# Performance work log

Hardware: AMD Instinct MI355X
Metric: run time of the kernel (lower is better)

## Reference

```python
import jax, jax.numpy as jnp
import numpy as np

GROUPS = 32
N_HEADS = 8
EPS = 1e-5


def setup_inputs() -> dict:
    key = jax.random.key(0)
    ks = jax.random.split(key, 4)
    B, C, H, W = 8, 512, 32, 32
    x = jax.random.normal(ks[0], (B, C, H, W), dtype=jnp.float32)
    norm_scale = jnp.ones((C,), jnp.float32)
    norm_bias = jnp.zeros((C,), jnp.float32)
    qkv_w = jax.random.normal(ks[1], (3 * C, C), jnp.float32) * (C ** -0.5)
    qkv_b = jnp.zeros((3 * C,), jnp.float32)
    proj_w = jax.random.normal(ks[2], (C, C), jnp.float32) * (C ** -0.5)
    proj_b = jnp.zeros((C,), jnp.float32)
    return {"x": x, "norm_scale": norm_scale, "norm_bias": norm_bias,
            "qkv_w": qkv_w, "qkv_b": qkv_b, "proj_w": proj_w, "proj_b": proj_b}


def reference(x, norm_scale, norm_bias, qkv_w, qkv_b, proj_w, proj_b):
    B, C, H, W = x.shape
    T = H * W
    xf = x.reshape(B, C, T)

    # GroupNorm32 (32 groups, computed in float32, affine)
    xg = xf.astype(jnp.float32).reshape(B, GROUPS, C // GROUPS, T)
    mean = xg.mean(axis=(2, 3), keepdims=True)
    var = xg.var(axis=(2, 3), keepdims=True)
    xn = ((xg - mean) * jax.lax.rsqrt(var + EPS)).reshape(B, C, T)
    xn = (xn * norm_scale[:, None] + norm_bias[:, None]).astype(x.dtype)

    # qkv: 1x1 conv1d == pointwise matmul -> [B, 3C, T]
    qkv = jnp.einsum('oc,bct->bot', qkv_w, xn) + qkv_b[:, None]

    # QKVAttentionLegacy: reshape to [B*H, 3*ch, T], split
    ch = C // N_HEADS
    qkv_h = qkv.reshape(B * N_HEADS, 3 * ch, T)
    q, k, v = qkv_h[:, :ch], qkv_h[:, ch:2 * ch], qkv_h[:, 2 * ch:]
    scale = ch ** -0.25
    weight = jnp.einsum('bct,bcs->bts', q * scale, k * scale)  # [B*H, T, T]
    weight = jax.nn.softmax(weight.astype(jnp.float32), axis=-1).astype(qkv.dtype)
    a = jnp.einsum('bts,bcs->bct', weight, v).reshape(B, C, T)

    # proj_out (1x1 conv) + residual
    h = jnp.einsum('oc,bct->bot', proj_w, a) + proj_b[:, None]
    return (xf + h).reshape(B, C, H, W)
```

## Files before the change

kernel.cpp:

```cpp
#include <hip/hip_runtime.h>
#include <hip/hip_bf16.h>
#include <stdint.h>

typedef unsigned short u16;
typedef unsigned int u32;
typedef __bf16 bf16x8 __attribute__((ext_vector_type(8)));
typedef float f32x4 __attribute__((ext_vector_type(4)));


static __device__ __forceinline__ u16 f2bf(float f) {
  union { __hip_bfloat16 h; u16 u; } c;
  c.h = __float2bfloat16(f);
  return c.u;
}

static __device__ __forceinline__ void gload_lds16(const void* g, void* l) {
  __builtin_amdgcn_global_load_lds(
      (__attribute__((address_space(1))) u32*)(uintptr_t)g,
      (__attribute__((address_space(3))) u32*)l, 16, 0, 0);
}

__global__ __launch_bounds__(256) void wcvt(const float* __restrict__ wq,
                                            const float* __restrict__ wp,
                                            u16* __restrict__ wqb,
                                            u16* __restrict__ wpb) {
  int idx = (blockIdx.x * 256 + threadIdx.x) * 4;
  const float* s;
  u16* d;
  if (idx < 786432) { s = wq + idx; d = wqb + idx; }
  else { int k = idx - 786432; s = wp + k; d = wpb + k; }
  float4 v = *(const float4*)s;
  uint2 o;
  o.x = (u32)f2bf(v.x) | ((u32)f2bf(v.y) << 16);
  o.y = (u32)f2bf(v.z) | ((u32)f2bf(v.w) << 16);
  *(uint2*)d = o;
}

__global__ __launch_bounds__(256) void gn_stats(const float* __restrict__ x,
                                                float* __restrict__ st) {
  int bg = blockIdx.x;
  const float* p = x + (size_t)bg * 16384;
  float s1 = 0.f, s2 = 0.f;
  for (int i = threadIdx.x * 4; i < 16384; i += 1024) {
    float4 v = *(const float4*)(p + i);
    s1 += v.x + v.y + v.z + v.w;
    s2 += v.x * v.x + v.y * v.y + v.z * v.z + v.w * v.w;
  }
#pragma unroll
  for (int off = 1; off < 64; off <<= 1) {
    s1 += __shfl_xor(s1, off);
    s2 += __shfl_xor(s2, off);
  }
  __shared__ float r1[4], r2[4];
  int w = threadIdx.x >> 6, l = threadIdx.x & 63;
  if (l == 0) { r1[w] = s1; r2[w] = s2; }
  __syncthreads();
  if (threadIdx.x == 0) {
    float t1 = r1[0] + r1[1] + r1[2] + r1[3];
    float t2 = r2[0] + r2[1] + r2[2] + r2[3];
    float mean = t1 * (1.f / 16384.f);
    float var = t2 * (1.f / 16384.f) - mean * mean;
    st[bg * 2] = mean;
    st[bg * 2 + 1] = rsqrtf(var + 1e-5f);
  }
}

__global__ __launch_bounds__(256) void gn_apply(const float* __restrict__ x,
                                                const float* __restrict__ st,
                                                const float* __restrict__ ns,
                                                const float* __restrict__ nbi,
                                                u16* __restrict__ xnt) {
  __shared__ u16 tile[32 * 520];
  int b = blockIdx.x >> 5;
  int t0 = (blockIdx.x & 31) << 5;
  int tid = threadIdx.x;
  int tl = tid & 31, cg = tid >> 5;
#pragma unroll 4
  for (int cc = 0; cc < 64; ++cc) {
    int c = cc * 8 + cg;
    float mean = st[(b * 32 + (c >> 4)) * 2];
    float rstd = st[(b * 32 + (c >> 4)) * 2 + 1];
    float v = x[(size_t)b * 524288 + (size_t)c * 1024 + t0 + tl];
    float vn = (v - mean) * rstd * ns[c] + nbi[c];
    tile[tl * 520 + c] = f2bf(vn);
  }
  __syncthreads();
#pragma unroll
  for (int i = 0; i < 8; ++i) {
    int chunk = i * 256 + tid;
    int tl2 = chunk >> 6;
    int c0 = (chunk & 63) * 8;
    uint4 d = *(const uint4*)(tile + tl2 * 520 + c0);
    *(uint4*)(xnt + (size_t)b * 524288 + (size_t)(t0 + tl2) * 512 + c0) = d;
  }
}

static __device__ __forceinline__ void gemm_core(const u16* Abase, const u16* Bbase,
                                                 f32x4 acc[4][4], u16* As, u16* Bs,
                                                 int w, int l, int wm, int wn) {
  const int r8 = l >> 3, ch = l & 7;
  const int fr = l & 15, fq = l >> 4;
#pragma unroll 1
  for (int kt = 0; kt < 8; ++kt) {
    __syncthreads();
#pragma unroll
    for (int i = 0; i < 4; ++i) {
      int gi = (w << 2) + i;
      int row = (gi << 3) + r8;
      int xoff = ((ch ^ (row & 7)) << 4);
      gload_lds16((const char*)Abase + (size_t)row * 1024 + (kt << 7) + xoff,
                  (char*)As + (gi << 10));
      gload_lds16((const char*)Bbase + (size_t)row * 1024 + (kt << 7) + xoff,
                  (char*)Bs + (gi << 10));
    }
    __syncthreads();
#pragma unroll
    for (int kf = 0; kf < 2; ++kf) {
      bf16x8 af[4], bfv[4];
#pragma unroll
      for (int i = 0; i < 4; ++i) {
        int rowA = wm * 64 + i * 16 + fr;
        af[i] = *(const bf16x8*)(As + rowA * 64 + ((((kf << 2) + fq) ^ (rowA & 7)) << 3));
        int rowB = wn * 64 + i * 16 + fr;
        bfv[i] = *(const bf16x8*)(Bs + rowB * 64 + ((((kf << 2) + fq) ^ (rowB & 7)) << 3));
      }
#pragma unroll
      for (int i = 0; i < 4; ++i)
#pragma unroll
        for (int j = 0; j < 4; ++j)
          acc[i][j] = __builtin_amdgcn_mfma_f32_16x16x32_bf16(af[i], bfv[j], acc[i][j], 0, 0, 0);
    }
  }
}

__global__ __launch_bounds__(256) void gemm_qkv(const u16* __restrict__ Wq,
                                                const u16* __restrict__ Xnt,
                                                const float* __restrict__ bq,
                                                u16* __restrict__ qT,
                                                u16* __restrict__ kT,
                                                u16* __restrict__ vv) {
  __shared__ u16 SMEM[18432];
  int bid0 = blockIdx.x;
  int bid = (bid0 & 7) * 96 + (bid0 >> 3);
  int mb = bid % 12, nb = (bid / 12) % 8, b = bid / 96;
  int tid = threadIdx.x, w = tid >> 6, l = tid & 63;
  int wm = tid >> 7, wn = (tid >> 6) & 1;
  int fr = l & 15, fq = l >> 4;
  f32x4 acc[4][4];
#pragma unroll
  for (int i = 0; i < 4; ++i)
#pragma unroll
    for (int j = 0; j < 4; ++j) acc[i][j] = (f32x4){0.f, 0.f, 0.f, 0.f};

  gemm_core(Wq + (size_t)mb * 65536, Xnt + (size_t)b * 524288 + (size_t)nb * 65536,
            acc, SMEM, SMEM + 8192, w, l, wm, wn);

  __syncthreads();

  int seg2 = mb * 2 + wm;
  int h = seg2 / 3, typ = seg2 % 3;
  size_t hb = (size_t)(b * 8 + h) * 65536;
  u16* SUB = SMEM + wm * 9216;

  if (typ < 2) {
    float qksc = (typ == 0) ? 0.51011687f : 0.35355339f;
#pragma unroll
    for (int i = 0; i < 4; ++i) {
      int oi = i * 16 + fq * 4;
      float4 bb = *(const float4*)(bq + mb * 128 + wm * 64 + oi);
#pragma unroll
      for (int j = 0; j < 4; ++j) {
        int tl = wn * 64 + j * 16 + fr;
        f32x4 v = acc[i][j];
        u32 lo = (u32)f2bf((v[0] + bb.x) * qksc) | ((u32)f2bf((v[1] + bb.y) * qksc) << 16);
        u32 hi = (u32)f2bf((v[2] + bb.z) * qksc) | ((u32)f2bf((v[3] + bb.w) * qksc) << 16);
        *(u32*)(SUB + tl * 72 + oi) = lo;
        *(u32*)(SUB + tl * 72 + oi + 2) = hi;
      }
    }
  } else {
#pragma unroll
    for (int i = 0; i < 4; ++i) {
      int oi = i * 16 + fq * 4;
      float4 bb = *(const float4*)(bq + mb * 128 + wm * 64 + oi);
      float bbv[4] = {bb.x, bb.y, bb.z, bb.w};
#pragma unroll
      for (int j = 0; j < 4; ++j) {
        int tl = wn * 64 + j * 16 + fr;
        f32x4 v = acc[i][j];
#pragma unroll
        for (int r = 0; r < 4; ++r)
          SUB[(oi + r) * 136 + tl] = f2bf(v[r] + bbv[r]);
      }
    }
  }
  __syncthreads();

  int lt = tid & 127;
  if (typ < 2) {
    u16* dstb = (typ == 0 ? qT : kT) + hb;
#pragma unroll
    for (int it = 0; it < 8; ++it) {
      int slot = it * 128 + lt;
      int t = slot >> 3, chk = slot & 7;
      uint4 val = *(const uint4*)(SUB + t * 72 + chk * 8);
      *(uint4*)(dstb + (size_t)(nb * 128 + t) * 64 + chk * 8) = val;
    }
  } else {
#pragma unroll
    for (int it = 0; it < 8; ++it) {
      int slot = it * 128 + lt;
      int c = slot >> 4, chk = slot & 15;
      uint4 val = *(const uint4*)(SUB + c * 136 + chk * 8);
      *(uint4*)(vv + hb + (size_t)c * 1024 + nb * 128 + chk * 8) = val;
    }
  }
}

__global__ __launch_bounds__(512) void attn(const u16* __restrict__ qT,
                                            const u16* __restrict__ kT,
                                            const u16* __restrict__ vv,
                                            u16* __restrict__ aT) {
  __shared__ u16 Ks[64 * 64];
  __shared__ u16 Vs[80 * 64];
  __shared__ u16 Ps[8 * 16 * 72];
  int bid = blockIdx.x;
  int bh = (bid & 7) * 8 + (bid >> 6);
  int tq = (bid >> 3) & 7;
  int tid = threadIdx.x, w = tid >> 6, l = tid & 63;
  int fr = l & 15, fq = l >> 4;
  int r8 = l >> 3, ch = l & 7;
  size_t hb = (size_t)bh * 65536;

  {
    int row = 64 + (tid >> 5);
    int c2 = (tid & 31) * 2;
    u16 val = (row == 64) ? (u16)0x3F80 : (u16)0;
    Vs[row * 64 + c2] = val;
    Vs[row * 64 + c2 + 1] = val;
  }

  bf16x8 aq[2];
  {
    const u16* qp = qT + hb + (size_t)(tq * 128 + w * 16 + fr) * 64 + fq * 8;
    aq[0] = *(const bf16x8*)(qp);
    aq[1] = *(const bf16x8*)(qp + 32);
  }

  f32x4 acc_o[4];
  f32x4 acc_s = (f32x4){0.f, 0.f, 0.f, 0.f};
#pragma unroll
  for (int nb = 0; nb < 4; ++nb) acc_o[nb] = (f32x4){0.f, 0.f, 0.f, 0.f};

  u16* pw = Ps + w * (16 * 72);

  for (int st = 0; st < 16; ++st) {
    __syncthreads();
    {
      int row = (w << 3) + r8;
      int xoff = ((ch ^ (row & 7)) << 4);
      gload_lds16((const char*)(kT + hb) + (size_t)(st * 64 + row) * 128 + xoff,
                  (char*)Ks + (w << 10));
      gload_lds16((const char*)(vv + hb) + (size_t)row * 2048 + st * 128 + xoff,
                  (char*)Vs + (w << 10));
    }
    __syncthreads();

    f32x4 sa[4];
#pragma unroll
    for (int nb = 0; nb < 4; ++nb) sa[nb] = (f32x4){0.f, 0.f, 0.f, 0.f};
    __builtin_amdgcn_s_setprio(1);
#pragma unroll
    for (int nb = 0; nb < 4; ++nb) {
      int krow = nb * 16 + fr;
#pragma unroll
      for (int kf = 0; kf < 2; ++kf) {
        bf16x8 bk = *(const bf16x8*)(Ks + krow * 64 + ((((kf << 2) + fq) ^ (krow & 7)) << 3));
        sa[nb] = __builtin_amdgcn_mfma_f32_16x16x32_bf16(aq[kf], bk, sa[nb], 0, 0, 0);
      }
    }
    __builtin_amdgcn_s_setprio(0);

#pragma unroll
    for (int nb = 0; nb < 4; ++nb)
#pragma unroll
      for (int r = 0; r < 4; ++r)
        pw[(fq * 4 + r) * 72 + nb * 16 + fr] = f2bf(exp2f(sa[nb][r]));

    bf16x8 ap[2];
#pragma unroll
    for (int kf = 0; kf < 2; ++kf)
      ap[kf] = *(const bf16x8*)(pw + fr * 72 + kf * 32 + fq * 8);

    __builtin_amdgcn_s_setprio(1);
#pragma unroll
    for (int nb = 0; nb < 4; ++nb) {
      int vrow = nb * 16 + fr;
#pragma unroll
      for (int kf = 0; kf < 2; ++kf) {
        bf16x8 bv = *(const bf16x8*)(Vs + vrow * 64 + ((((kf << 2) + fq) ^ (vrow & 7)) << 3));
        acc_o[nb] = __builtin_amdgcn_mfma_f32_16x16x32_bf16(ap[kf], bv, acc_o[nb], 0, 0, 0);
      }
    }
    {
      int vrow = 64 + fr;
#pragma unroll
      for (int kf = 0; kf < 2; ++kf) {
        bf16x8 bv = *(const bf16x8*)(Vs + vrow * 64 + ((((kf << 2) + fq) ^ (vrow & 7)) << 3));
        acc_s = __builtin_amdgcn_mfma_f32_16x16x32_bf16(ap[kf], bv, acc_s, 0, 0, 0);
      }
    }
    __builtin_amdgcn_s_setprio(0);
  }

  int b = bh >> 3, h = bh & 7;
  f32x4 invl;
#pragma unroll
  for (int r = 0; r < 4; ++r) invl[r] = 1.f / __shfl(acc_s[r], l & 48);
#pragma unroll
  for (int nb = 0; nb < 4; ++nb) {
    f32x4 ov = acc_o[nb] * invl;
#pragma unroll
    for (int r = 0; r < 4; ++r) {
      int t = tq * 128 + w * 16 + fq * 4 + r;
      aT[(size_t)b * 524288 + (size_t)t * 512 + h * 64 + nb * 16 + fr] = f2bf(ov[r]);
    }
  }
}

__global__ __launch_bounds__(256) void gemm_proj(const u16* __restrict__ Wp,
                                                 const u16* __restrict__ aT,
                                                 const float* __restrict__ bp,
                                                 const float* __restrict__ x,
                                                 float* __restrict__ out) {
  __shared__ u16 As[128 * 64];
  __shared__ u16 Bs[128 * 64];
  int bid0 = blockIdx.x;
  int bid = (bid0 & 7) * 32 + (bid0 >> 3);
  int mb = bid & 3, nb = (bid >> 2) & 7, b = bid >> 5;
  int tid = threadIdx.x, w = tid >> 6, l = tid & 63;
  int wm = w >> 1, wn = w & 1;
  f32x4 acc[4][4];
#pragma unroll
  for (int i = 0; i < 4; ++i)
#pragma unroll
    for (int j = 0; j < 4; ++j) acc[i][j] = (f32x4){0.f, 0.f, 0.f, 0.f};

  gemm_core(Wp + (size_t)mb * 65536, aT + (size_t)b * 524288 + (size_t)nb * 65536,
            acc, As, Bs, w, l, wm, wn);

  int fr = l & 15, fq = l >> 4;
#pragma unroll
  for (int i = 0; i < 4; ++i) {
    int o0 = mb * 128 + wm * 64 + i * 16 + fq * 4;
    float b0 = bp[o0], b1 = bp[o0 + 1], b2 = bp[o0 + 2], b3 = bp[o0 + 3];
#pragma unroll
    for (int j = 0; j < 4; ++j) {
      int t = nb * 128 + wn * 64 + j * 16 + fr;
      f32x4 v = acc[i][j];
      size_t base = (size_t)b * 524288 + (size_t)o0 * 1024 + t;
      out[base] = x[base] + v[0] + b0;
      out[base + 1024] = x[base + 1024] + v[1] + b1;
      out[base + 2048] = x[base + 2048] + v[2] + b2;
      out[base + 3072] = x[base + 3072] + v[3] + b3;
    }
  }
}

extern "C" void kernel_launch(void* const* d_in, const int* in_sizes, int n_in,
                              void* d_out, int out_size, void* d_ws, size_t ws_size,
                              hipStream_t stream) {
  const float* x = (const float*)d_in[0];
  const float* ns = (const float*)d_in[1];
  const float* nbi = (const float*)d_in[2];
  const float* wq = (const float*)d_in[3];
  const float* bq = (const float*)d_in[4];
  const float* wp = (const float*)d_in[5];
  const float* bp = (const float*)d_in[6];
  float* out = (float*)d_out;
  char* ws = (char*)d_ws;

  u16* wqb = (u16*)(ws);
  u16* wpb = (u16*)(ws + 1572864);
  float* st = (float*)(ws + 2097152);
  u16* xnt = (u16*)(ws + 2101248);
  u16* qT = (u16*)(ws + 2101248 + 8388608);
  u16* kT = (u16*)(ws + 2101248 + 2 * 8388608);
  u16* vv = (u16*)(ws + 2101248 + 3 * 8388608);
  u16* aT = xnt;

  hipLaunchKernelGGL(wcvt, dim3(1024), dim3(256), 0, stream, wq, wp, wqb, wpb);
  hipLaunchKernelGGL(gn_stats, dim3(256), dim3(256), 0, stream, x, st);
  hipLaunchKernelGGL(gn_apply, dim3(256), dim3(256), 0, stream, x, st, ns, nbi, xnt);
  hipLaunchKernelGGL(gemm_qkv, dim3(768), dim3(256), 0, stream, wqb, xnt, bq, qT, kT, vv);
  hipLaunchKernelGGL(attn, dim3(512), dim3(512), 0, stream, qT, kT, vv, aT);
  hipLaunchKernelGGL(gemm_proj, dim3(256), dim3(256), 0, stream, wpb, aT, bp, x, out);
}
```

Baseline: 95.96 us.

## Load K/V fragments directly from global memory instead of staging through LDS

The attention kernel stops cooperatively staging K and V tiles into shared memory with block-wide barriers. Each wave now reads its MFMA operand fragments straight from global memory, relying on L1/L2 caching across the eight waves. The row-sum is computed with a constant all-ones register operand instead of an LDS padding row, which removes the shuffle in the epilogue. This drops two __syncthreads per iteration but adds redundant per-wave global loads, and the loop is forced not to unroll.

Measured after the change: 179.2 us. 1.87x slower.

```diff
diff --git a/kernel.cpp b/kernel.cpp
--- a/kernel.cpp
+++ b/kernel.cpp
@@ -221,24 +221,13 @@
                                             const u16* __restrict__ kT,
                                             const u16* __restrict__ vv,
                                             u16* __restrict__ aT) {
-  __shared__ u16 Ks[64 * 64];
-  __shared__ u16 Vs[80 * 64];
   __shared__ u16 Ps[8 * 16 * 72];
   int bid = blockIdx.x;
   int bh = (bid & 7) * 8 + (bid >> 6);
   int tq = (bid >> 3) & 7;
   int tid = threadIdx.x, w = tid >> 6, l = tid & 63;
   int fr = l & 15, fq = l >> 4;
-  int r8 = l >> 3, ch = l & 7;
   size_t hb = (size_t)bh * 65536;
-
-  {
-    int row = 64 + (tid >> 5);
-    int c2 = (tid & 31) * 2;
-    u16 val = (row == 64) ? (u16)0x3F80 : (u16)0;
-    Vs[row * 64 + c2] = val;
-    Vs[row * 64 + c2 + 1] = val;
-  }
 
   bf16x8 aq[2];
   {
@@ -246,6 +235,13 @@
     aq[0] = *(const bf16x8*)(qp);
     aq[1] = *(const bf16x8*)(qp + 32);
   }
+  const u16* kb = kT + hb + (size_t)fr * 64 + fq * 8;
+  const u16* vb = vv + hb + (size_t)fr * 1024 + fq * 8;
+
+  union { u32 u[4]; bf16x8 v; } onesu;
+#pragma unroll
+  for (int i = 0; i < 4; ++i) onesu.u[i] = 0x3F803F80u;
+  const bf16x8 vone = onesu.v;
 
   f32x4 acc_o[4];
   f32x4 acc_s = (f32x4){0.f, 0.f, 0.f, 0.f};
@@ -254,28 +250,17 @@
 
   u16* pw = Ps + w * (16 * 72);
 
+#pragma unroll 1
   for (int st = 0; st < 16; ++st) {
-    __syncthreads();
-    {
-      int row = (w << 3) + r8;
-      int xoff = ((ch ^ (row & 7)) << 4);
-      gload_lds16((const char*)(kT + hb) + (size_t)(st * 64 + row) * 128 + xoff,
-                  (char*)Ks + (w << 10));
-      gload_lds16((const char*)(vv + hb) + (size_t)row * 2048 + st * 128 + xoff,
-                  (char*)Vs + (w << 10));
-    }
-    __syncthreads();
-
     f32x4 sa[4];
 #pragma unroll
     for (int nb = 0; nb < 4; ++nb) sa[nb] = (f32x4){0.f, 0.f, 0.f, 0.f};
     __builtin_amdgcn_s_setprio(1);
 #pragma unroll
     for (int nb = 0; nb < 4; ++nb) {
-      int krow = nb * 16 + fr;
 #pragma unroll
       for (int kf = 0; kf < 2; ++kf) {
-        bf16x8 bk = *(const bf16x8*)(Ks + krow * 64 + ((((kf << 2) + fq) ^ (krow & 7)) << 3));
+        bf16x8 bk = *(const bf16x8*)(kb + (size_t)(st * 64 + nb * 16) * 64 + kf * 32);
         sa[nb] = __builtin_amdgcn_mfma_f32_16x16x32_bf16(aq[kf], bk, sa[nb], 0, 0, 0);
       }
     }
@@ -295,28 +280,22 @@
     __builtin_amdgcn_s_setprio(1);
 #pragma unroll
     for (int nb = 0; nb < 4; ++nb) {
-      int vrow = nb * 16 + fr;
 #pragma unroll
       for (int kf = 0; kf < 2; ++kf) {
-        bf16x8 bv = *(const bf16x8*)(Vs + vrow * 64 + ((((kf << 2) + fq) ^ (vrow & 7)) << 3));
+        bf16x8 bv = *(const bf16x8*)(vb + (size_t)(nb * 16) * 1024 + st * 64 + kf * 32);
         acc_o[nb] = __builtin_amdgcn_mfma_f32_16x16x32_bf16(ap[kf], bv, acc_o[nb], 0, 0, 0);
       }
     }
-    {
-      int vrow = 64 + fr;
-#pragma unroll
-      for (int kf = 0; kf < 2; ++kf) {
-        bf16x8 bv = *(const bf16x8*)(Vs + vrow * 64 + ((((kf << 2) + fq) ^ (vrow & 7)) << 3));
-        acc_s = __builtin_amdgcn_mfma_f32_16x16x32_bf16(ap[kf], bv, acc_s, 0, 0, 0);
-      }
-    }
+#pragma unroll
+    for (int kf = 0; kf < 2; ++kf)
+      acc_s = __builtin_amdgcn_mfma_f32_16x16x32_bf16(ap[kf], vone, acc_s, 0, 0, 0);
     __builtin_amdgcn_s_setprio(0);
   }
 
   int b = bh >> 3, h = bh & 7;
   f32x4 invl;
 #pragma unroll
-  for (int r = 0; r < 4; ++r) invl[r] = 1.f / __shfl(acc_s[r], l & 48);
+  for (int r = 0; r < 4; ++r) invl[r] = 1.f / acc_s[r];
 #pragma unroll
   for (int nb = 0; nb < 4; ++nb) {
     f32x4 ov = acc_o[nb] * invl;
```
